# Optimization experiments

Hardware: AMD Instinct MI355X
Metric: run time of the kernel (lower is better)

Reference implementation:

```python
import jax, jax.numpy as jnp
import numpy as np

N, D, H, O = 200000, 256, 256, 128


def _linear_params(key, fan_in, fan_out):
    # matches torch.nn.Linear default init: U(-1/sqrt(fan_in), 1/sqrt(fan_in))
    lim = 1.0 / np.sqrt(fan_in)
    kw, kb = jax.random.split(key)
    W = jax.random.uniform(kw, (fan_in, fan_out), minval=-lim, maxval=lim, dtype=jnp.float32)
    b = jax.random.uniform(kb, (fan_out,), minval=-lim, maxval=lim, dtype=jnp.float32)
    return W, b


def setup_inputs() -> dict:
    key = jax.random.key(0)
    ks = jax.random.split(key, 6)
    node_embeddings = jax.random.normal(ks[0], (N, D), dtype=jnp.float32)
    # adjacency_list keys: all < N so every key is 'valid'
    adj_keys = jax.random.randint(ks[1], (N,), 0, N, dtype=jnp.int64) if jax.config.jax_enable_x64 else jax.random.randint(ks[1], (N,), 0, N, dtype=jnp.int32)
    W1, b1 = _linear_params(ks[2], D, H)
    W2, b2 = _linear_params(ks[3], H, H)
    W3, b3 = _linear_params(ks[4], H, H)
    Wo, bo = _linear_params(ks[5], H, O)
    return {
        "node_embeddings": node_embeddings,
        "adj_keys": adj_keys,
        "W1": W1, "b1": b1,
        "W2": W2, "b2": b2,
        "W3": W3, "b3": b3,
        "Wo": Wo, "bo": bo,
    }


def reference(node_embeddings, adj_keys, W1, b1, W2, b2, W3, b3, Wo, bo):
    # --- aggregation path (faithful to the torch code's actual math) ---
    # All adj_keys are < N, so valid_indices == keys and the re-enumeration
    # `mapping` makes `indices` exactly arange(num_keys).
    indices = jnp.arange(adj_keys.shape[0])
    neighbors = node_embeddings[indices]              # [N, D] row gather
    # torch.mean(row, dim=0) on a 1-D row == scalar mean over features
    aggregated_embeddings = jnp.mean(neighbors, axis=1)  # [N]

    # --- dense 3-layer SAGE MLP + output projection ---
    x = jax.nn.relu(node_embeddings @ W1 + b1)        # [N, H]
    x = jax.nn.relu(x @ W2 + b2)                      # [N, H]
    x = jax.nn.relu(x @ W3 + b3)                      # [N, H]
    x = x @ Wo + bo                                   # [N, O]
    return (x, aggregated_embeddings)
```

## Files before the change

kernel.cpp:

```cpp
#include <hip/hip_runtime.h>
#include <hip/hip_bf16.h>
#include <cstdint>


#define N_ROWS 200000
#define O_DIM  128
#define ROWS   128
#define PITCH  264

typedef short bf16x8 __attribute__((ext_vector_type(8)));
typedef float f32x4  __attribute__((ext_vector_type(4)));

__device__ __forceinline__ unsigned short rne_bf16(float f) {
  unsigned int u = __float_as_uint(f);
  u += 0x7FFFu + ((u >> 16) & 1u);
  return (unsigned short)(u >> 16);
}

__global__ __launch_bounds__(256) void prep_kernel(
    const float* __restrict__ W1, const float* __restrict__ W2,
    const float* __restrict__ W3, const float* __restrict__ Wo,
    unsigned short* __restrict__ wt) {
  const int b = blockIdx.x;
  const int t = threadIdx.x;
  if (b < 256) {
    wt[b * 256 + t] = rne_bf16(W1[t * 256 + b]);
  } else if (b < 512) {
    const int o = b - 256;
    wt[65536 + o * 256 + t] = rne_bf16(W2[t * 256 + o]);
  } else if (b < 768) {
    const int o = b - 512;
    wt[131072 + o * 256 + t] = rne_bf16(W3[t * 256 + o]);
  } else {
    const int o = b - 768;
    wt[196608 + o * 256 + t] = rne_bf16(Wo[t * 128 + o]);
  }
}

template <int MB, bool RELU, bool LAST>
__device__ __forceinline__ void do_layer(
    const unsigned short* __restrict__ wt, const float* __restrict__ bias,
    float* __restrict__ out_x, long row0, unsigned short* act,
    int wave, int lane) {
  const int lc   = lane & 15;
  const int quad = lane >> 4;
  const int m_base = wave * (MB * 16);

  f32x4 acc[MB][8];
#pragma unroll
  for (int mb = 0; mb < MB; ++mb)
#pragma unroll
    for (int nb = 0; nb < 8; ++nb)
      acc[mb][nb] = (f32x4){0.f, 0.f, 0.f, 0.f};

#pragma unroll
  for (int k0 = 0; k0 < 256; k0 += 32) {
    bf16x8 bfr[8];
#pragma unroll
    for (int nb = 0; nb < 8; ++nb)
      bfr[nb] = *(const bf16x8*)&act[(nb * 16 + lc) * PITCH + k0 + 8 * quad];
#pragma unroll
    for (int mb = 0; mb < MB; ++mb) {
      bf16x8 afr = *(const bf16x8*)&wt[(m_base + mb * 16 + lc) * 256 + k0 + 8 * quad];
#pragma unroll
      for (int nb = 0; nb < 8; ++nb)
        acc[mb][nb] = __builtin_amdgcn_mfma_f32_16x16x32_bf16(afr, bfr[nb],
                                                              acc[mb][nb], 0, 0, 0);
    }
  }
  __syncthreads();

#pragma unroll
  for (int mb = 0; mb < MB; ++mb) {
    const int ch = m_base + mb * 16 + 4 * quad;
    f32x4 bb = *(const f32x4*)(bias + ch);
#pragma unroll
    for (int nb = 0; nb < 8; ++nb) {
      f32x4 v = acc[mb][nb] + bb;
      if (RELU) {
#pragma unroll
        for (int j = 0; j < 4; ++j) v[j] = fmaxf(v[j], 0.f);
      }
      const int r = nb * 16 + lc;
      if (!LAST) {
        ushort4 h;
        h.x = rne_bf16(v[0]); h.y = rne_bf16(v[1]);
        h.z = rne_bf16(v[2]); h.w = rne_bf16(v[3]);
        *(ushort4*)&act[r * PITCH + ch] = h;
      } else {
        const long gr = row0 + r;
        if (gr < N_ROWS) *(f32x4*)&out_x[gr * O_DIM + ch] = v;
      }
    }
  }
  __syncthreads();
}

__global__ __launch_bounds__(256, 2) void sage_kernel(
    const float* __restrict__ E,
    const float* __restrict__ b1, const float* __restrict__ b2,
    const float* __restrict__ b3, const float* __restrict__ bo,
    const unsigned short* __restrict__ wts,
    float* __restrict__ out_x, float* __restrict__ out_agg) {
  __shared__ __align__(16) unsigned short act[ROWS * PITCH];

  const int t    = threadIdx.x;
  const int wave = t >> 6;
  const int lane = t & 63;
  const long row0 = (long)blockIdx.x * ROWS;

#pragma unroll 4
  for (int i = 0; i < 32; ++i) {
    const int r = 4 * i + wave;
    const long gr = row0 + r;
    f32x4 v = (f32x4){0.f, 0.f, 0.f, 0.f};
    if (gr < N_ROWS) v = *(const f32x4*)(E + gr * 256 + lane * 4);
    ushort4 h;
    h.x = rne_bf16(v[0]); h.y = rne_bf16(v[1]);
    h.z = rne_bf16(v[2]); h.w = rne_bf16(v[3]);
    *(ushort4*)&act[r * PITCH + lane * 4] = h;
    float s = v[0] + v[1] + v[2] + v[3];
    s += __shfl_down(s, 32);
    s += __shfl_down(s, 16);
    s += __shfl_down(s, 8);
    s += __shfl_down(s, 4);
    s += __shfl_down(s, 2);
    s += __shfl_down(s, 1);
    if (lane == 0 && gr < N_ROWS) out_agg[gr] = s * (1.0f / 256.0f);
  }
  __syncthreads();

  do_layer<4, true,  false>(wts,          b1, nullptr, row0, act, wave, lane);
  do_layer<4, true,  false>(wts + 65536,  b2, nullptr, row0, act, wave, lane);
  do_layer<4, true,  false>(wts + 131072, b3, nullptr, row0, act, wave, lane);
  do_layer<2, false, true >(wts + 196608, bo, out_x,   row0, act, wave, lane);
}

extern "C" void kernel_launch(void* const* d_in, const int* in_sizes, int n_in,
                              void* d_out, int out_size, void* d_ws, size_t ws_size,
                              hipStream_t stream) {
  const float* E  = (const float*)d_in[0];
  const float* W1 = (const float*)d_in[2];
  const float* b1 = (const float*)d_in[3];
  const float* W2 = (const float*)d_in[4];
  const float* b2 = (const float*)d_in[5];
  const float* W3 = (const float*)d_in[6];
  const float* b3 = (const float*)d_in[7];
  const float* Wo = (const float*)d_in[8];
  const float* bo = (const float*)d_in[9];

  float* out_x   = (float*)d_out;
  float* out_agg = out_x + (size_t)N_ROWS * O_DIM;
  unsigned short* wts = (unsigned short*)d_ws;

  prep_kernel<<<896, 256, 0, stream>>>(W1, W2, W3, Wo, wts);

  const int grid = (N_ROWS + ROWS - 1) / ROWS;
  sage_kernel<<<grid, 256, 0, stream>>>(E, b1, b2, b3, bo, wts, out_x, out_agg);
}
```

Baseline: 512.4 us.

## Halve row tile to 64, raise occupancy, tile-transpose weight prep

Reduces rows per block from 128 to 64, which halves the LDS activation buffer and the accumulator registers, and raises the launch bound to 4 blocks per SM so more waves can hide memory latency. Bounds checks are dropped because 200000 divides evenly by 64. The weight prep kernel now transposes through a 64x64 shared-memory tile so both its reads and writes are coalesced, using 56 blocks instead of 896. In exchange, each weight fragment loaded from global/L2 is reused across fewer rows, so weight traffic per row doubles.

```diff
diff --git a/kernel.cpp b/kernel.cpp
--- a/kernel.cpp
+++ b/kernel.cpp
@@ -5,7 +5,7 @@
 
 #define N_ROWS 200000
 #define O_DIM  128
-#define ROWS   128
+#define ROWS   64
 #define PITCH  264
 
 typedef short bf16x8 __attribute__((ext_vector_type(8)));
@@ -21,19 +21,30 @@
     const float* __restrict__ W1, const float* __restrict__ W2,
     const float* __restrict__ W3, const float* __restrict__ Wo,
     unsigned short* __restrict__ wt) {
+  __shared__ float tile[64][65];
   const int b = blockIdx.x;
-  const int t = threadIdx.x;
-  if (b < 256) {
-    wt[b * 256 + t] = rne_bf16(W1[t * 256 + b]);
-  } else if (b < 512) {
-    const int o = b - 256;
-    wt[65536 + o * 256 + t] = rne_bf16(W2[t * 256 + o]);
-  } else if (b < 768) {
-    const int o = b - 512;
-    wt[131072 + o * 256 + t] = rne_bf16(W3[t * 256 + o]);
-  } else {
-    const int o = b - 768;
-    wt[196608 + o * 256 + t] = rne_bf16(Wo[t * 128 + o]);
+  int which, tb;
+  if (b < 48) { which = b >> 4; tb = b & 15; }
+  else        { which = 3;      tb = b - 48; }
+  const float* W = (which == 0) ? W1 : (which == 1) ? W2 : (which == 2) ? W3 : Wo;
+  const int O = (which == 3) ? 128 : 256;
+  unsigned short* out = wt + (size_t)which * 65536;
+  const int otiles = O >> 6;
+  const int r0 = (tb / otiles) * 64;
+  const int c0 = (tb % otiles) * 64;
+
+  const int j  = threadIdx.x & 63;
+  const int ib = threadIdx.x >> 6;
+#pragma unroll
+  for (int ii = 0; ii < 16; ++ii) {
+    const int i = ii * 4 + ib;
+    tile[i][j] = W[(size_t)(r0 + i) * O + c0 + j];
+  }
+  __syncthreads();
+#pragma unroll
+  for (int ii = 0; ii < 16; ++ii) {
+    const int i = ii * 4 + ib;
+    out[(size_t)(c0 + i) * 256 + r0 + j] = rne_bf16(tile[j][i]);
   }
 }
 
@@ -45,25 +56,26 @@
   const int lc   = lane & 15;
   const int quad = lane >> 4;
   const int m_base = wave * (MB * 16);
+  constexpr int NB = ROWS / 16;
 
-  f32x4 acc[MB][8];
+  f32x4 acc[MB][NB];
 #pragma unroll
   for (int mb = 0; mb < MB; ++mb)
 #pragma unroll
-    for (int nb = 0; nb < 8; ++nb)
+    for (int nb = 0; nb < NB; ++nb)
       acc[mb][nb] = (f32x4){0.f, 0.f, 0.f, 0.f};
 
 #pragma unroll
   for (int k0 = 0; k0 < 256; k0 += 32) {
-    bf16x8 bfr[8];
+    bf16x8 bfr[NB];
 #pragma unroll
-    for (int nb = 0; nb < 8; ++nb)
+    for (int nb = 0; nb < NB; ++nb)
       bfr[nb] = *(const bf16x8*)&act[(nb * 16 + lc) * PITCH + k0 + 8 * quad];
 #pragma unroll
     for (int mb = 0; mb < MB; ++mb) {
       bf16x8 afr = *(const bf16x8*)&wt[(m_base + mb * 16 + lc) * 256 + k0 + 8 * quad];
 #pragma unroll
-      for (int nb = 0; nb < 8; ++nb)
+      for (int nb = 0; nb < NB; ++nb)
         acc[mb][nb] = __builtin_amdgcn_mfma_f32_16x16x32_bf16(afr, bfr[nb],
                                                               acc[mb][nb], 0, 0, 0);
     }
@@ -75,7 +87,7 @@
     const int ch = m_base + mb * 16 + 4 * quad;
     f32x4 bb = *(const f32x4*)(bias + ch);
 #pragma unroll
-    for (int nb = 0; nb < 8; ++nb) {
+    for (int nb = 0; nb < NB; ++nb) {
       f32x4 v = acc[mb][nb] + bb;
       if (RELU) {
 #pragma unroll
@@ -88,15 +100,14 @@
         h.z = rne_bf16(v[2]); h.w = rne_bf16(v[3]);
         *(ushort4*)&act[r * PITCH + ch] = h;
       } else {
-        const long gr = row0 + r;
-        if (gr < N_ROWS) *(f32x4*)&out_x[gr * O_DIM + ch] = v;
+        *(f32x4*)&out_x[(row0 + r) * O_DIM + ch] = v;
       }
     }
   }
   __syncthreads();
 }
 
-__global__ __launch_bounds__(256, 2) void sage_kernel(
+__global__ __launch_bounds__(256, 4) void sage_kernel(
     const float* __restrict__ E,
     const float* __restrict__ b1, const float* __restrict__ b2,
     const float* __restrict__ b3, const float* __restrict__ bo,
@@ -109,12 +120,11 @@
   const int lane = t & 63;
   const long row0 = (long)blockIdx.x * ROWS;
 
-#pragma unroll 4
-  for (int i = 0; i < 32; ++i) {
+#pragma unroll
+  for (int i = 0; i < ROWS / 4; ++i) {
     const int r = 4 * i + wave;
     const long gr = row0 + r;
-    f32x4 v = (f32x4){0.f, 0.f, 0.f, 0.f};
-    if (gr < N_ROWS) v = *(const f32x4*)(E + gr * 256 + lane * 4);
+    f32x4 v = *(const f32x4*)(E + gr * 256 + lane * 4);
     ushort4 h;
     h.x = rne_bf16(v[0]); h.y = rne_bf16(v[1]);
     h.z = rne_bf16(v[2]); h.w = rne_bf16(v[3]);
@@ -126,7 +136,7 @@
     s += __shfl_down(s, 4);
     s += __shfl_down(s, 2);
     s += __shfl_down(s, 1);
-    if (lane == 0 && gr < N_ROWS) out_agg[gr] = s * (1.0f / 256.0f);
+    if (lane == 0) out_agg[gr] = s * (1.0f / 256.0f);
   }
   __syncthreads();
 
@@ -153,8 +163,8 @@
   float* out_agg = out_x + (size_t)N_ROWS * O_DIM;
   unsigned short* wts = (unsigned short*)d_ws;
 
-  prep_kernel<<<896, 256, 0, stream>>>(W1, W2, W3, Wo, wts);
+  prep_kernel<<<56, 256, 0, stream>>>(W1, W2, W3, Wo, wts);
 
-  const int grid = (N_ROWS + ROWS - 1) / ROWS;
+  const int grid = N_ROWS / ROWS;
   sage_kernel<<<grid, 256, 0, stream>>>(E, b1, b2, b3, bo, wts, out_x, out_agg);
 }
```

Result: slower. 540.6 us (+5.5%).
